# Kernel optimization log

Hardware: AMD Instinct MI355X
Metric: run time of the kernel (lower is better)

The kernel has to match this reference:

```python
import jax, jax.numpy as jnp
import numpy as np

B, N, E = 128, 196, 2048   # batch, num_features (14x14), encoder_dim
D, A = 512, 512            # decoder_dim, attention_dim


def setup_inputs() -> dict:
    key = jax.random.key(0)
    ks = jax.random.split(key, 8)
    s_e = 1.0 / np.sqrt(E)
    s_d = 1.0 / np.sqrt(D)
    s_a = 1.0 / np.sqrt(A)
    return {
        "encoder_out": jax.random.normal(ks[0], (B, N, E), dtype=jnp.float32),
        "decoder_hidden": jax.random.normal(ks[1], (B, D), dtype=jnp.float32),
        "We": jax.random.uniform(ks[2], (E, A), jnp.float32, -s_e, s_e),
        "be": jax.random.uniform(ks[3], (A,), jnp.float32, -s_e, s_e),
        "Wd": jax.random.uniform(ks[4], (D, A), jnp.float32, -s_d, s_d),
        "bd": jax.random.uniform(ks[5], (A,), jnp.float32, -s_d, s_d),
        "Wf": jax.random.uniform(ks[6], (A, 1), jnp.float32, -s_a, s_a),
        "bf": jax.random.uniform(ks[7], (1,), jnp.float32, -s_a, s_a),
    }


def reference(encoder_out, decoder_hidden, We, be, Wd, bd, Wf, bf):
    # att1: [B,N,A] projection of encoder features
    att1 = jnp.einsum('bne,ea->bna', encoder_out, We) + be
    # att2: [B,A] projection of decoder state, broadcast over N
    att2 = decoder_hidden @ Wd + bd
    att = jnp.tanh(att1 + att2[:, None, :])          # [B,N,A]
    scores = jnp.einsum('bna,ao->bno', att, Wf) + bf  # [B,N,1]
    alpha = jax.nn.softmax(scores, axis=1)            # softmax over num_features
    context = jnp.sum(encoder_out * alpha, axis=1)    # [B,E]
    return (context, alpha)
```

## Files before the change

### kernel.cpp

```cpp
#include <hip/hip_runtime.h>
#include <hip/hip_bf16.h>
#include <stdint.h>

#define B_   128
#define N_   196
#define E_   2048
#define D_   512
#define A_   512
#define MTOT (B_ * N_)

typedef short  short8  __attribute__((ext_vector_type(8)));
typedef float  floatx4 __attribute__((ext_vector_type(4)));

__device__ __forceinline__ unsigned short f2bf(float f) {
    union { float f; uint32_t u; } v; v.f = f;
    uint32_t r = v.u + 0x7FFFu + ((v.u >> 16) & 1u);
    return (unsigned short)(r >> 16);
}

__device__ __forceinline__ uint32_t pkbf(float a, float b) {
    uint32_t ua = __float_as_uint(a) + 0x8000u;
    uint32_t ub = __float_as_uint(b) + 0x8000u;
    return __builtin_amdgcn_perm(ub, ua, 0x07060302u);
}

__global__ void transcvt_k(const float* __restrict__ We, unsigned short* __restrict__ WeT) {
    __shared__ float tile[32][33];
    const int e0 = blockIdx.x * 32, a0 = blockIdx.y * 32;
    const int t = threadIdx.x, tc = t & 31, tr = t >> 5;
#pragma unroll
    for (int i = 0; i < 4; ++i) {
        int r = tr + i * 8;
        tile[r][tc] = We[(size_t)(e0 + r) * A_ + a0 + tc];
    }
    __syncthreads();
#pragma unroll
    for (int i = 0; i < 4; ++i) {
        int r = tr + i * 8;
        WeT[(size_t)(a0 + r) * E_ + e0 + tc] = f2bf(tile[tc][r]);
    }
}

__launch_bounds__(512)
__global__ void att2_k(const float* __restrict__ dh, const float* __restrict__ Wd,
                       const float* __restrict__ bd, const float* __restrict__ be,
                       float* __restrict__ att2p) {
    const int b = blockIdx.x, t = threadIdx.x;
    __shared__ float sdh[D_];
    sdh[t] = dh[b * D_ + t];
    __syncthreads();
    float acc = 0.f;
#pragma unroll 8
    for (int d = 0; d < D_; ++d) acc += sdh[d] * Wd[(size_t)d * A_ + t];
    att2p[(size_t)b * A_ + t] = acc + bd[t] + be[t];
}

__launch_bounds__(512, 6)
__global__ void score_gemm(const float* __restrict__ enc,
                           const unsigned short* __restrict__ WeT,
                           const float* __restrict__ att2p,
                           const float* __restrict__ Wf,
                           float* __restrict__ scoresP) {
    __shared__ __align__(16) char sMem[2 * 20480];
    __shared__ float sPart[8][64];

    const int t   = threadIdx.x;
    const int w   = t >> 6;
    const int l   = t & 63;
    const int l15 = l & 15;
    const int q4  = l >> 4;
    const int rowBlk = blockIdx.x >> 1;
    const int half   = blockIdx.x & 1;
    const int row0   = rowBlk * 64;
    const int col0   = half * 256;

    floatx4 acc[4][2] = {};

    const int ar = t >> 3, ap = t & 7;
    const float* aSrcT = enc + (size_t)(row0 + ar) * E_ + ap * 4;
    const int aWr = ar * 64 + (((ap >> 1) ^ ((ar >> 1) & 3)) * 16) + (ap & 1) * 8;

    const unsigned short* bSrc[2];
    int bDst[2];
#pragma unroll
    for (int j = 0; j < 2; ++j) {
        int s = w * 2 + j;
        int n = s * 16 + (l >> 2), p = l & 3;
        int q = p ^ ((n >> 1) & 3);
        bSrc[j] = WeT + (size_t)(col0 + n) * E_ + q * 8;
        bDst[j] = 4096 + s * 1024;
    }

    const int chA  = q4 ^ ((l15 >> 1) & 3);
    const int offA = l15 * 64 + chA * 16;
    const int offB = 4096 + (w * 32 + l15) * 64 + chA * 16;

    {
        float4 a0 = *(const float4*)(aSrcT);
#pragma unroll
        for (int j = 0; j < 2; ++j)
            __builtin_amdgcn_global_load_lds(
                (const __attribute__((address_space(1))) uint32_t*)(bSrc[j]),
                (__attribute__((address_space(3))) uint32_t*)(sMem + bDst[j]), 16, 0, 0);
        uint2 aw;
        aw.x = pkbf(a0.x, a0.y);
        aw.y = pkbf(a0.z, a0.w);
        *(uint2*)(sMem + aWr) = aw;
        __syncthreads();
    }

    int cur = 0;
#pragma unroll 2
    for (int kk = 0; kk < 64; ++kk) {
        const int nxt = cur ^ 20480;
        const int kn  = (kk + 1) & 63;

        float4 aNext = *(const float4*)(aSrcT + kn * 32);
#pragma unroll
        for (int j = 0; j < 2; ++j)
            __builtin_amdgcn_global_load_lds(
                (const __attribute__((address_space(1))) uint32_t*)(bSrc[j] + kn * 32),
                (__attribute__((address_space(3))) uint32_t*)(sMem + nxt + bDst[j]), 16, 0, 0);

        short8 bfr[2];
#pragma unroll
        for (int ni = 0; ni < 2; ++ni)
            bfr[ni] = *(const short8*)(sMem + cur + offB + ni * 1024);
#pragma unroll
        for (int mi = 0; mi < 4; ++mi) {
            short8 a = *(const short8*)(sMem + cur + offA + mi * 1024);
            acc[mi][0] = __builtin_amdgcn_mfma_f32_16x16x32_bf16(a, bfr[0], acc[mi][0], 0, 0, 0);
            acc[mi][1] = __builtin_amdgcn_mfma_f32_16x16x32_bf16(a, bfr[1], acc[mi][1], 0, 0, 0);
        }

        uint2 aw;
        aw.x = pkbf(aNext.x, aNext.y);
        aw.y = pkbf(aNext.z, aNext.w);
        *(uint2*)(sMem + nxt + aWr) = aw;
        __syncthreads();
        cur = nxt;
    }

    const int cbase = col0 + w * 32;
    float wfv[2];
#pragma unroll
    for (int ni = 0; ni < 2; ++ni) wfv[ni] = Wf[cbase + ni * 16 + l15];

#pragma unroll
    for (int mi = 0; mi < 4; ++mi) {
#pragma unroll
        for (int r = 0; r < 4; ++r) {
            const int m    = mi * 16 + q4 * 4 + r;
            const int grow = row0 + m;
            const int bb   = grow / N_;
            const float* a2 = att2p + (size_t)bb * A_ + cbase;
            float s = 0.f;
#pragma unroll
            for (int ni = 0; ni < 2; ++ni) {
                float v  = acc[mi][ni][r] + a2[ni * 16 + l15];
                float e  = __expf(2.f * v);
                float th = 1.f - 2.f / (e + 1.f);
                s += th * wfv[ni];
            }
            s += __shfl_xor(s, 1);
            s += __shfl_xor(s, 2);
            s += __shfl_xor(s, 4);
            s += __shfl_xor(s, 8);
            if (l15 == 0) sPart[w][m] = s;
        }
    }
    __syncthreads();
    if (t < 64) {
        float v = 0.f;
#pragma unroll
        for (int ww = 0; ww < 8; ++ww) v += sPart[ww][t];
        scoresP[(size_t)half * MTOT + row0 + t] = v;
    }
}

__launch_bounds__(256)
__global__ void ctx_sm_k(const float* __restrict__ enc, const float* __restrict__ sp,
                         float* __restrict__ alpha, float* __restrict__ ctx) {
    const int chunk = blockIdx.x, b = blockIdx.y;
    const int t = threadIdx.x, w = t >> 6, l = t & 63;
    const int tn = t >> 6, tc = t & 63;
    __shared__ float  sAl[N_];
    __shared__ float  red[8];
    __shared__ float4 sRed[256];

    float v = -3.0e38f;
    if (t < N_) v = sp[b * N_ + t] + sp[MTOT + b * N_ + t];
    float m = v;
#pragma unroll
    for (int off = 32; off >= 1; off >>= 1) m = fmaxf(m, __shfl_xor(m, off));
    if (l == 0) red[w] = m;
    __syncthreads();
    m = fmaxf(fmaxf(red[0], red[1]), fmaxf(red[2], red[3]));
    float e = 0.f;
    if (t < N_) e = __expf(v - m);
    float s = e;
#pragma unroll
    for (int off = 32; off >= 1; off >>= 1) s += __shfl_xor(s, off);
    if (l == 0) red[4 + w] = s;
    __syncthreads();
    s = red[4] + red[5] + red[6] + red[7];
    if (t < N_) {
        float al = e / s;
        sAl[t] = al;
        if (chunk == 0) alpha[b * N_ + t] = al;
    }
    __syncthreads();

    const float* base = enc + (size_t)b * N_ * E_ + chunk * 256 + tc * 4;
    float4 a = make_float4(0.f, 0.f, 0.f, 0.f);
#pragma unroll 7
    for (int n = tn; n < N_; n += 4) {
        float  al = sAl[n];
        float4 vv = *(const float4*)(base + (size_t)n * E_);
        a.x += al * vv.x; a.y += al * vv.y; a.z += al * vv.z; a.w += al * vv.w;
    }
    sRed[t] = a;
    __syncthreads();
    if (t < 64) {
        float4 r0 = sRed[t], r1 = sRed[t + 64], r2 = sRed[t + 128], r3 = sRed[t + 192];
        float4 o = make_float4(r0.x + r1.x + r2.x + r3.x, r0.y + r1.y + r2.y + r3.y,
                               r0.z + r1.z + r2.z + r3.z, r0.w + r1.w + r2.w + r3.w);
        *(float4*)(ctx + (size_t)b * E_ + chunk * 256 + t * 4) = o;
    }
}

extern "C" void kernel_launch(void* const* d_in, const int* in_sizes, int n_in,
                              void* d_out, int out_size, void* d_ws, size_t ws_size,
                              hipStream_t stream) {
    const float* enc = (const float*)d_in[0];
    const float* dh  = (const float*)d_in[1];
    const float* We  = (const float*)d_in[2];
    const float* be  = (const float*)d_in[3];
    const float* Wd  = (const float*)d_in[4];
    const float* bd  = (const float*)d_in[5];
    const float* Wf  = (const float*)d_in[6];

    float* out   = (float*)d_out;
    float* ctx   = out;
    float* alpha = out + B_ * E_;

    char* ws = (char*)d_ws;
    unsigned short* WeT  = (unsigned short*)ws;
    float* att2p         = (float*)(ws + (2u << 20));
    float* scoresP       = (float*)(ws + (2u << 20) + (256u << 10));

    transcvt_k <<<dim3(E_ / 32, A_ / 32), 256, 0, stream>>>(We, WeT);
    att2_k     <<<dim3(B_),              512, 0, stream>>>(dh, Wd, bd, be, att2p);
    score_gemm <<<dim3(2 * MTOT / 64),   512, 0, stream>>>(enc, WeT, att2p, Wf, scoresP);
    ctx_sm_k   <<<dim3(E_ / 256, B_),    256, 0, stream>>>(enc, scoresP, alpha, ctx);
}
```

Measured before the change: 479.8 us.

## Retile score GEMM to 128x128 blocks with 2x2 waves and XCD-aware block mapping

The fused score GEMM moves from 64x256 tiles on 512 threads to 128x128 tiles on 256 threads. Each wave now computes a 64x64 sub-tile with a 4x4 MFMA accumulator grid, which raises register reuse of the A and B fragments. Blocks are remapped so the four column blocks of one row strip land on the same XCD, so the encoder rows re-read across column blocks should mostly hit L2. The trade-off is that the score partials are split four ways instead of two, so the softmax kernel sums four partial buffers. The encoder data is also fetched and converted to bf16 four times instead of twice, and the larger accumulator set raises register pressure.

Result: faster. 441.2 us (-8.0%).

```diff
diff --git a/kernel.cpp b/kernel.cpp
--- a/kernel.cpp
+++ b/kernel.cpp
@@ -55,30 +55,34 @@
     att2p[(size_t)b * A_ + t] = acc + bd[t] + be[t];
 }
 
-__launch_bounds__(512, 6)
+__launch_bounds__(256, 4)
 __global__ void score_gemm(const float* __restrict__ enc,
                            const unsigned short* __restrict__ WeT,
                            const float* __restrict__ att2p,
                            const float* __restrict__ Wf,
                            float* __restrict__ scoresP) {
-    __shared__ __align__(16) char sMem[2 * 20480];
-    __shared__ float sPart[8][64];
+    __shared__ __align__(16) char sMem[2 * 16384];
+    __shared__ float sPart[2][128];
 
     const int t   = threadIdx.x;
     const int w   = t >> 6;
     const int l   = t & 63;
     const int l15 = l & 15;
     const int q4  = l >> 4;
-    const int rowBlk = blockIdx.x >> 1;
-    const int half   = blockIdx.x & 1;
-    const int row0   = rowBlk * 64;
-    const int col0   = half * 256;
-
-    floatx4 acc[4][2] = {};
-
-    const int ar = t >> 3, ap = t & 7;
-    const float* aSrcT = enc + (size_t)(row0 + ar) * E_ + ap * 4;
-    const int aWr = ar * 64 + (((ap >> 1) ^ ((ar >> 1) & 3)) * 16) + (ap & 1) * 8;
+    const int wr  = w >> 1, wc = w & 1;
+
+    const int v     = (blockIdx.x & 7) * 98 + (blockIdx.x >> 3);
+    const int strip = v >> 2, colb = v & 3;
+    const int row0  = strip * 128;
+    const int c0    = colb * 128;
+
+    floatx4 acc[4][4] = {};
+
+    const int ar = t >> 1, ah = t & 1;
+    const float* aSrcT = enc + (size_t)(row0 + ar) * E_ + ah * 16;
+    const int aswz = (ar >> 1) & 3;
+    const int aWr0 = ar * 64 + (((2 * ah)     ^ aswz) * 16);
+    const int aWr1 = ar * 64 + (((2 * ah + 1) ^ aswz) * 16);
 
     const unsigned short* bSrc[2];
     int bDst[2];
@@ -87,78 +91,92 @@
         int s = w * 2 + j;
         int n = s * 16 + (l >> 2), p = l & 3;
         int q = p ^ ((n >> 1) & 3);
-        bSrc[j] = WeT + (size_t)(col0 + n) * E_ + q * 8;
-        bDst[j] = 4096 + s * 1024;
-    }
-
-    const int chA  = q4 ^ ((l15 >> 1) & 3);
-    const int offA = l15 * 64 + chA * 16;
-    const int offB = 4096 + (w * 32 + l15) * 64 + chA * 16;
+        bSrc[j] = WeT + (size_t)(c0 + n) * E_ + q * 8;
+        bDst[j] = 8192 + s * 1024;
+    }
+
+    const int chR  = q4 ^ ((l15 >> 1) & 3);
+    const int offA = (wr * 64 + l15) * 64 + chR * 16;
+    const int offB = 8192 + (wc * 64 + l15) * 64 + chR * 16;
 
     {
         float4 a0 = *(const float4*)(aSrcT);
+        float4 a1 = *(const float4*)(aSrcT + 4);
+        float4 a2 = *(const float4*)(aSrcT + 8);
+        float4 a3 = *(const float4*)(aSrcT + 12);
 #pragma unroll
         for (int j = 0; j < 2; ++j)
             __builtin_amdgcn_global_load_lds(
                 (const __attribute__((address_space(1))) uint32_t*)(bSrc[j]),
                 (__attribute__((address_space(3))) uint32_t*)(sMem + bDst[j]), 16, 0, 0);
-        uint2 aw;
-        aw.x = pkbf(a0.x, a0.y);
-        aw.y = pkbf(a0.z, a0.w);
-        *(uint2*)(sMem + aWr) = aw;
+        uint4 w0, w1;
+        w0.x = pkbf(a0.x, a0.y); w0.y = pkbf(a0.z, a0.w);
+        w0.z = pkbf(a1.x, a1.y); w0.w = pkbf(a1.z, a1.w);
+        w1.x = pkbf(a2.x, a2.y); w1.y = pkbf(a2.z, a2.w);
+        w1.z = pkbf(a3.x, a3.y); w1.w = pkbf(a3.z, a3.w);
+        *(uint4*)(sMem + aWr0) = w0;
+        *(uint4*)(sMem + aWr1) = w1;
         __syncthreads();
     }
 
     int cur = 0;
 #pragma unroll 2
     for (int kk = 0; kk < 64; ++kk) {
-        const int nxt = cur ^ 20480;
+        const int nxt = cur ^ 16384;
         const int kn  = (kk + 1) & 63;
 
-        float4 aNext = *(const float4*)(aSrcT + kn * 32);
+        float4 a0 = *(const float4*)(aSrcT + kn * 32);
+        float4 a1 = *(const float4*)(aSrcT + kn * 32 + 4);
+        float4 a2 = *(const float4*)(aSrcT + kn * 32 + 8);
+        float4 a3 = *(const float4*)(aSrcT + kn * 32 + 12);
 #pragma unroll
         for (int j = 0; j < 2; ++j)
             __builtin_amdgcn_global_load_lds(
                 (const __attribute__((address_space(1))) uint32_t*)(bSrc[j] + kn * 32),
                 (__attribute__((address_space(3))) uint32_t*)(sMem + nxt + bDst[j]), 16, 0, 0);
 
-        short8 bfr[2];
-#pragma unroll
-        for (int ni = 0; ni < 2; ++ni)
+        short8 bfr[4];
+#pragma unroll
+        for (int ni = 0; ni < 4; ++ni)
             bfr[ni] = *(const short8*)(sMem + cur + offB + ni * 1024);
 #pragma unroll
         for (int mi = 0; mi < 4; ++mi) {
             short8 a = *(const short8*)(sMem + cur + offA + mi * 1024);
             acc[mi][0] = __builtin_amdgcn_mfma_f32_16x16x32_bf16(a, bfr[0], acc[mi][0], 0, 0, 0);
             acc[mi][1] = __builtin_amdgcn_mfma_f32_16x16x32_bf16(a, bfr[1], acc[mi][1], 0, 0, 0);
+            acc[mi][2] = __builtin_amdgcn_mfma_f32_16x16x32_bf16(a, bfr[2], acc[mi][2], 0, 0, 0);
+            acc[mi][3] = __builtin_amdgcn_mfma_f32_16x16x32_bf16(a, bfr[3], acc[mi][3], 0, 0, 0);
         }
 
-        uint2 aw;
-        aw.x = pkbf(aNext.x, aNext.y);
-        aw.y = pkbf(aNext.z, aNext.w);
-        *(uint2*)(sMem + nxt + aWr) = aw;
+        uint4 w0, w1;
+        w0.x = pkbf(a0.x, a0.y); w0.y = pkbf(a0.z, a0.w);
+        w0.z = pkbf(a1.x, a1.y); w0.w = pkbf(a1.z, a1.w);
+        w1.x = pkbf(a2.x, a2.y); w1.y = pkbf(a2.z, a2.w);
+        w1.z = pkbf(a3.x, a3.y); w1.w = pkbf(a3.z, a3.w);
+        *(uint4*)(sMem + nxt + aWr0) = w0;
+        *(uint4*)(sMem + nxt + aWr1) = w1;
         __syncthreads();
         cur = nxt;
     }
 
-    const int cbase = col0 + w * 32;
-    float wfv[2];
-#pragma unroll
-    for (int ni = 0; ni < 2; ++ni) wfv[ni] = Wf[cbase + ni * 16 + l15];
+    const int cbase = c0 + wc * 64;
+    float wfv[4];
+#pragma unroll
+    for (int ni = 0; ni < 4; ++ni) wfv[ni] = Wf[cbase + ni * 16 + l15];
 
 #pragma unroll
     for (int mi = 0; mi < 4; ++mi) {
 #pragma unroll
         for (int r = 0; r < 4; ++r) {
-            const int m    = mi * 16 + q4 * 4 + r;
+            const int m    = wr * 64 + mi * 16 + q4 * 4 + r;
             const int grow = row0 + m;
             const int bb   = grow / N_;
-            const float* a2 = att2p + (size_t)bb * A_ + cbase;
+            const float* a2p = att2p + (size_t)bb * A_ + cbase;
             float s = 0.f;
 #pragma unroll
-            for (int ni = 0; ni < 2; ++ni) {
-                float v  = acc[mi][ni][r] + a2[ni * 16 + l15];
-                float e  = __expf(2.f * v);
+            for (int ni = 0; ni < 4; ++ni) {
+                float vv = acc[mi][ni][r] + a2p[ni * 16 + l15];
+                float e  = __expf(2.f * vv);
                 float th = 1.f - 2.f / (e + 1.f);
                 s += th * wfv[ni];
             }
@@ -166,15 +184,12 @@
             s += __shfl_xor(s, 2);
             s += __shfl_xor(s, 4);
             s += __shfl_xor(s, 8);
-            if (l15 == 0) sPart[w][m] = s;
+            if (l15 == 0) sPart[wc][m] = s;
         }
     }
     __syncthreads();
-    if (t < 64) {
-        float v = 0.f;
-#pragma unroll
-        for (int ww = 0; ww < 8; ++ww) v += sPart[ww][t];
-        scoresP[(size_t)half * MTOT + row0 + t] = v;
+    if (t < 128) {
+        scoresP[(size_t)colb * MTOT + row0 + t] = sPart[0][t] + sPart[1][t];
     }
 }
 
@@ -189,7 +204,10 @@
     __shared__ float4 sRed[256];
 
     float v = -3.0e38f;
-    if (t < N_) v = sp[b * N_ + t] + sp[MTOT + b * N_ + t];
+    if (t < N_) {
+        const int i = b * N_ + t;
+        v = sp[i] + sp[MTOT + i] + sp[2 * MTOT + i] + sp[3 * MTOT + i];
+    }
     float m = v;
 #pragma unroll
     for (int off = 32; off >= 1; off >>= 1) m = fmaxf(m, __shfl_xor(m, off));
@@ -251,6 +269,6 @@
 
     transcvt_k <<<dim3(E_ / 32, A_ / 32), 256, 0, stream>>>(We, WeT);
     att2_k     <<<dim3(B_),              512, 0, stream>>>(dh, Wd, bd, be, att2p);
-    score_gemm <<<dim3(2 * MTOT / 64),   512, 0, stream>>>(enc, WeT, att2p, Wf, scoresP);
+    score_gemm <<<dim3(4 * MTOT / 128),  256, 0, stream>>>(enc, WeT, att2p, Wf, scoresP);
     ctx_sm_k   <<<dim3(E_ / 256, B_),    256, 0, stream>>>(enc, scoresP, alpha, ctx);
 }
```
